# Kernel tuning notes

Hardware: AMD Instinct MI355X
Metric: run time of the kernel (lower is better)

The kernel has to match this reference:

```python
import jax, jax.numpy as jnp
import numpy as np

N, E, R = 50000, 1600000, 8
IN_F, HID_F, OUT_F = 128, 64, 64


def setup_inputs() -> dict:
    key = jax.random.key(0)
    ks = jax.random.split(key, 9)
    x = jax.random.normal(ks[0], (N, IN_F), dtype=jnp.float32)
    edge_index = jax.random.randint(ks[1], (2, E), 0, N, dtype=jnp.int64)
    edge_type = jax.random.randint(ks[2], (E,), 0, R, dtype=jnp.int64)
    # layer 1 params (scaled like glorot)
    s1 = 1.0 / np.sqrt(IN_F)
    W1_rel = jax.random.normal(ks[3], (R, IN_F, HID_F), dtype=jnp.float32) * s1
    W1_root = jax.random.normal(ks[4], (IN_F, HID_F), dtype=jnp.float32) * s1
    b1 = jnp.zeros((HID_F,), dtype=jnp.float32)
    # layer 2 params
    s2 = 1.0 / np.sqrt(HID_F)
    W2_rel = jax.random.normal(ks[5], (R, HID_F, OUT_F), dtype=jnp.float32) * s2
    W2_root = jax.random.normal(ks[6], (HID_F, OUT_F), dtype=jnp.float32) * s2
    b2 = jnp.zeros((OUT_F,), dtype=jnp.float32)
    return {"x": x, "edge_index": edge_index, "edge_type": edge_type,
            "W1_rel": W1_rel, "W1_root": W1_root, "b1": b1,
            "W2_rel": W2_rel, "W2_root": W2_root, "b2": b2}


def _rgcn_conv(x, src, dst, etype, W_rel, W_root, b):
    """PyG RGCNConv: root transform + per-relation mean-aggregated messages."""
    n = x.shape[0]
    r = W_rel.shape[0]
    # per-relation transform of all node features: [R, N, H]
    xw = jnp.einsum('nd,rdh->rnh', x, W_rel)
    # per-edge message: transformed source feature under the edge's relation
    msg = xw[etype, src]  # [E, H]
    # mean normalization per (dst, relation) pair
    key = dst * r + etype  # [E]
    cnt = jax.ops.segment_sum(jnp.ones(etype.shape, dtype=x.dtype), key,
                              num_segments=n * r)
    inv = 1.0 / jnp.maximum(cnt, 1.0)
    msg = msg * inv[key][:, None]
    # scatter-add into target nodes
    agg = jax.ops.segment_sum(msg, dst, num_segments=n)  # [N, H]
    return agg + x @ W_root + b


def reference(x, edge_index, edge_type, W1_rel, W1_root, b1, W2_rel, W2_root, b2):
    src, dst = edge_index[0], edge_index[1]
    h = _rgcn_conv(x, src, dst, edge_type, W1_rel, W1_root, b1)
    h = jax.nn.relu(h)
    out = _rgcn_conv(h, src, dst, edge_type, W2_rel, W2_root, b2)
    return out
```

## Files before the change

kernel.cpp:

```cpp
#include <hip/hip_runtime.h>


constexpr int NN  = 50000;
constexpr int NE  = 1600000;
constexpr int NR  = 8;
constexpr int FIN = 128;
constexpr int FH  = 64;

constexpr int BSH = 7;
constexpr int BN  = 1 << BSH;
constexpr int NB  = (NN + BN - 1) >> BSH;
constexpr int CAP = 6144;
constexpr int CH  = 4096;
constexpr unsigned XWMAX = (unsigned)(NN - 1) * (NR * 64) + (NR - 1) * 64;

typedef __attribute__((ext_vector_type(8))) short bf16x8;
typedef __attribute__((ext_vector_type(4))) float f32x4;

__device__ __forceinline__ unsigned short f2bf(float f) {
  unsigned u = __float_as_uint(f);
  u = (u + 0x7fff + ((u >> 16) & 1)) >> 16;
  return (unsigned short)u;
}
__device__ __forceinline__ float bf2f(unsigned short b) {
  return __uint_as_float(((unsigned)b) << 16);
}
__device__ __forceinline__ bool edge_ok(unsigned s, unsigned d, unsigned r) {
  return s < NN && d < NN && r < NR;
}

__global__ void __launch_bounds__(256) bucket_append(
    const int* __restrict__ src, const int* __restrict__ dst,
    const int* __restrict__ et, int* __restrict__ bcur,
    unsigned* __restrict__ brecs) {
  __shared__ uint2 stage[CH];
  __shared__ int h[NB], gbase[NB], sbase[NB], scur[NB];
  __shared__ int wtot[4];
  const int t  = threadIdx.x;
  const int c0 = blockIdx.x * CH;
  const int m  = min(CH, NE - c0);

  for (int i = t; i < NB; i += 256) h[i] = 0;
  __syncthreads();

  for (int i = t; i < m; i += 256) {
    const unsigned s = (unsigned)src[c0 + i];
    const unsigned d = (unsigned)dst[c0 + i];
    const unsigned r = (unsigned)et[c0 + i];
    if (edge_ok(s, d, r)) atomicAdd(&h[d >> BSH], 1);
  }
  __syncthreads();

  const int v0 = (2 * t < NB) ? h[2 * t] : 0;
  const int v1 = (2 * t + 1 < NB) ? h[2 * t + 1] : 0;
  if (2 * t < NB     && v0) gbase[2 * t]     = atomicAdd(&bcur[2 * t], v0);
  if (2 * t + 1 < NB && v1) gbase[2 * t + 1] = atomicAdd(&bcur[2 * t + 1], v1);
  const int s = v0 + v1;
  int incl = s;
#pragma unroll
  for (int o = 1; o < 64; o <<= 1) {
    int u = __shfl_up(incl, o, 64);
    if ((t & 63) >= o) incl += u;
  }
  if ((t & 63) == 63) wtot[t >> 6] = incl;
  __syncthreads();
  int wo = 0;
  for (int w = 0; w < (t >> 6); ++w) wo += wtot[w];
  const int e = wo + incl - s;
  if (2 * t < NB)     { sbase[2 * t] = e;          scur[2 * t] = e; }
  if (2 * t + 1 < NB) { sbase[2 * t + 1] = e + v0; scur[2 * t + 1] = e + v0; }
  __syncthreads();

  for (int i = t; i < m; i += 256) {
    const unsigned sv = (unsigned)src[c0 + i];
    const unsigned d  = (unsigned)dst[c0 + i];
    const unsigned r  = (unsigned)et[c0 + i];
    if (edge_ok(sv, d, r)) {
      const int p = atomicAdd(&scur[d >> BSH], 1);
      if (p < CH) stage[p] = make_uint2((sv << 10) | (((unsigned)d & (BN - 1)) << 3) | r, d);
    }
  }
  __syncthreads();

  const int M = min(sbase[NB - 1] + h[NB - 1], CH);
  for (int j = t; j < M; j += 256) {
    const uint2 rec = stage[j];
    const int b = (int)(rec.y >> BSH);
    const int idx = min(gbase[b] + (j - sbase[b]), NB * CAP - 1);
    brecs[idx] = rec.x;
  }
}

__global__ void __launch_bounds__(256) bucket_finalize(
    const int* __restrict__ bcur, const unsigned* __restrict__ brecs,
    float* __restrict__ inv, int* __restrict__ row_start,
    int* __restrict__ deg, unsigned* __restrict__ recs) {
  const int b    = blockIdx.x;
  const int base = b * CAP;
  const int m    = min(bcur[b] - base, CAP);
  const int d0   = b << BSH;
  __shared__ int cnt[BN * NR];
  __shared__ int curs[BN * NR];
  __shared__ int wtot[4];
  const int t = threadIdx.x;

  for (int i = t; i < BN * NR; i += 256) cnt[i] = 0;
  __syncthreads();
  for (int i = t; i < m; i += 256) {
    const unsigned rec = brecs[base + i];
    const int dl = (int)((rec >> 3) & (BN - 1));
    const int r  = (int)(rec & 7);
    atomicAdd(&cnt[dl * NR + r], 1);
  }
  __syncthreads();

  const int c0 = cnt[t * 4], c1 = cnt[t * 4 + 1], c2 = cnt[t * 4 + 2], c3 = cnt[t * 4 + 3];
  const int s = c0 + c1 + c2 + c3;
  int incl = s;
#pragma unroll
  for (int o = 1; o < 64; o <<= 1) {
    int u = __shfl_up(incl, o, 64);
    if ((t & 63) >= o) incl += u;
  }
  if ((t & 63) == 63) wtot[t >> 6] = incl;
  __syncthreads();
  int wo = 0;
  for (int w = 0; w < (t >> 6); ++w) wo += wtot[w];
  const int e = wo + incl - s;
  curs[t * 4]     = e;
  curs[t * 4 + 1] = e + c0;
  curs[t * 4 + 2] = e + c0 + c1;
  curs[t * 4 + 3] = e + c0 + c1 + c2;
  __syncthreads();

  if (t < BN) {
    const int d = d0 + t;
    if (d < NN) {
      const int start = curs[t * NR];
      const int end   = (t == BN - 1) ? m : curs[(t + 1) * NR];
      row_start[d] = base + start;
      deg[d]       = end - start;
#pragma unroll
      for (int r = 0; r < NR; ++r)
        inv[d * NR + r] = 1.0f / fmaxf((float)cnt[t * NR + r], 1.0f);
    }
  }
  __syncthreads();

  for (int i = t; i < m; i += 256) {
    const unsigned rec = brecs[base + i];
    const int dl = (int)((rec >> 3) & (BN - 1));
    const int r  = (int)(rec & 7);
    const unsigned sv = rec >> 10;
    const int p  = atomicAdd(&curs[dl * NR + r], 1);
    recs[base + min(p, CAP - 1)] = (sv << 9) | ((unsigned)r << 6);
  }
}

__global__ void prep(const float* __restrict__ W1r, const float* __restrict__ W1o,
                     const float* __restrict__ W2r, const float* __restrict__ W2o,
                     unsigned short* __restrict__ Wt1,
                     unsigned short* __restrict__ Wt2,
                     int* __restrict__ bcur) {
  const int i  = blockIdx.x * blockDim.x + threadIdx.x;
  if (i < NB) bcur[i] = i * CAP;
  const int n1 = (NR + 1) * 64 * FIN;
  const int n2 = (NR + 1) * 64 * FH;
  if (i < n1) {
    const int g = i / (64 * FIN), rem = i % (64 * FIN);
    const int n = rem / FIN, k = rem % FIN;
    const float* W = (g < NR) ? (W1r + (size_t)g * FIN * 64) : W1o;
    Wt1[i] = f2bf(W[k * 64 + n]);
  } else if (i < n1 + n2) {
    const int j = i - n1;
    const int g = j / (64 * FH), rem = j % (64 * FH);
    const int n = rem / FH, k = rem % FH;
    const float* W = (g < NR) ? (W2r + (size_t)g * FH * 64) : W2o;
    Wt2[j] = f2bf(W[k * 64 + n]);
  }
}

template <int K, bool A_FP32>
__global__ void __launch_bounds__(256) gemm_mfma(
    const void* __restrict__ Av, const unsigned short* __restrict__ Wt,
    const float* __restrict__ bias,
    unsigned short* __restrict__ xw, float* __restrict__ root_out) {
  constexpr int KP  = K + 8;
  constexpr int NCH = 64 * (K / 8) / 256;
  __shared__ unsigned short As[64 * KP];
  __shared__ unsigned short Bs[2][64 * KP];
  const int n0  = blockIdx.x * 64;
  const int tid = threadIdx.x;

  if constexpr (A_FP32) {
    const float* A = (const float*)Av;
    for (int c = tid; c < 64 * (K / 8); c += 256) {
      const int row = c / (K / 8), kp = (c % (K / 8)) * 8;
      bf16x8 v = {};
      if (n0 + row < NN) {
        const float* p = A + (size_t)(n0 + row) * K + kp;
        const float4 f0 = *(const float4*)p;
        const float4 f1 = *(const float4*)(p + 4);
        v[0] = f2bf(f0.x); v[1] = f2bf(f0.y); v[2] = f2bf(f0.z); v[3] = f2bf(f0.w);
        v[4] = f2bf(f1.x); v[5] = f2bf(f1.y); v[6] = f2bf(f1.z); v[7] = f2bf(f1.w);
      }
      *(bf16x8*)(As + row * KP + kp) = v;
    }
  } else {
    const unsigned short* A = (const unsigned short*)Av;
    for (int c = tid; c < 64 * (K / 8); c += 256) {
      const int row = c / (K / 8), kp = (c % (K / 8)) * 8;
      bf16x8 v = {};
      if (n0 + row < NN) v = *(const bf16x8*)(A + (size_t)(n0 + row) * K + kp);
      *(bf16x8*)(As + row * KP + kp) = v;
    }
  }

  for (int c = 0; c < NCH; ++c) {
    const int idx = tid + c * 256;
    const int row = idx / (K / 8), kp = (idx % (K / 8)) * 8;
    *(bf16x8*)(Bs[0] + row * KP + kp) = *(const bf16x8*)(Wt + idx * 8);
  }
  __syncthreads();

  const int wave = tid >> 6, lane = tid & 63;
  const int i16 = lane & 15, quad = lane >> 4;
  const int r0 = wave * 16 + i16;

  for (int g = 0; g <= NR; ++g) {
    const int buf = g & 1;
    bf16x8 breg[NCH];
    if (g < NR) {
      const unsigned short* Wn = Wt + (size_t)(g + 1) * 64 * K;
#pragma unroll
      for (int c = 0; c < NCH; ++c) breg[c] = *(const bf16x8*)(Wn + (tid + c * 256) * 8);
    }

    f32x4 acc[4] = {};
#pragma unroll
    for (int kc = 0; kc < K / 32; ++kc) {
      const int k0 = kc * 32 + quad * 8;
      const bf16x8 a0 = *(const bf16x8*)(As + r0 * KP + k0);
      const bf16x8 b0 = *(const bf16x8*)(Bs[buf] + (i16)      * KP + k0);
      const bf16x8 b1 = *(const bf16x8*)(Bs[buf] + (i16 + 16) * KP + k0);
      const bf16x8 b2 = *(const bf16x8*)(Bs[buf] + (i16 + 32) * KP + k0);
      const bf16x8 b3 = *(const bf16x8*)(Bs[buf] + (i16 + 48) * KP + k0);
      acc[0] = __builtin_amdgcn_mfma_f32_16x16x32_bf16(a0, b0, acc[0], 0, 0, 0);
      acc[1] = __builtin_amdgcn_mfma_f32_16x16x32_bf16(a0, b1, acc[1], 0, 0, 0);
      acc[2] = __builtin_amdgcn_mfma_f32_16x16x32_bf16(a0, b2, acc[2], 0, 0, 0);
      acc[3] = __builtin_amdgcn_mfma_f32_16x16x32_bf16(a0, b3, acc[3], 0, 0, 0);
    }

    if (g < NR) {
#pragma unroll
      for (int c = 0; c < NCH; ++c) {
        const int idx = tid + c * 256;
        const int row = idx / (K / 8), kp = (idx % (K / 8)) * 8;
        *(bf16x8*)(Bs[buf ^ 1] + row * KP + kp) = breg[c];
      }
    }

    if (g < NR) {
#pragma unroll
      for (int reg = 0; reg < 4; ++reg) {
        const int n = n0 + wave * 16 + quad * 4 + reg;
        if (n >= NN) continue;
        unsigned short* p = xw + (size_t)n * (NR * 64) + g * 64 + i16;
#pragma unroll
        for (int ct = 0; ct < 4; ++ct) p[ct * 16] = f2bf(acc[ct][reg]);
      }
    } else {
      float bv[4];
#pragma unroll
      for (int ct = 0; ct < 4; ++ct) bv[ct] = bias[ct * 16 + i16];
#pragma unroll
      for (int reg = 0; reg < 4; ++reg) {
        const int n = n0 + wave * 16 + quad * 4 + reg;
        if (n >= NN) continue;
        float* p = root_out + (size_t)n * 64 + i16;
#pragma unroll
        for (int ct = 0; ct < 4; ++ct) p[ct * 16] = acc[ct][reg] + bv[ct];
      }
    }
    __syncthreads();
  }
}

template <bool RELU_BF16>
__global__ void __launch_bounds__(256) agg_csr(
    const int* __restrict__ row_start, const int* __restrict__ deg,
    const unsigned* __restrict__ offs, const unsigned short* __restrict__ xw,
    const float* __restrict__ inv, const float* __restrict__ root,
    float* __restrict__ out_f32, unsigned short* __restrict__ out_b16) {
  const int gid  = blockIdx.x * blockDim.x + threadIdx.x;
  const int lane = gid & 63;
  const int d    = gid >> 6;
  if (d >= NN) return;
  const int e  = lane >> 3;
  const int l8 = lane & 7;
  const int base = row_start[d];
  const int n    = deg[d];
  const float invv = inv[(d << 3) + l8];
  float a[8] = {};

  for (int c = 0; c < n; c += 64) {
    const int m = min(64, n - c);
    unsigned off = 0;
    if (lane < m) off = offs[base + c + lane];
    for (int j = 0; j < m; j += 16) {
      const int i0 = j + e, i1 = j + 8 + e;
      unsigned u0 = __shfl(off, i0 & 63, 64);
      unsigned u1 = __shfl(off, i1 & 63, 64);
      float s0 = __shfl(invv, (int)((u0 >> 6) & 7), 64);
      float s1 = __shfl(invv, (int)((u1 >> 6) & 7), 64);
      u0 = min(u0, XWMAX); u1 = min(u1, XWMAX);
      if (i0 >= m) s0 = 0.f;
      if (i1 >= m) s1 = 0.f;
      const bf16x8 v0 = *(const bf16x8*)(xw + u0 + l8 * 8);
      const bf16x8 v1 = *(const bf16x8*)(xw + u1 + l8 * 8);
#pragma unroll
      for (int q = 0; q < 8; ++q) a[q] += bf2f((unsigned short)v0[q]) * s0;
#pragma unroll
      for (int q = 0; q < 8; ++q) a[q] += bf2f((unsigned short)v1[q]) * s1;
    }
  }

#pragma unroll
  for (int q = 0; q < 8; ++q) {
    a[q] += __shfl_xor(a[q], 8, 64);
    a[q] += __shfl_xor(a[q], 16, 64);
    a[q] += __shfl_xor(a[q], 32, 64);
  }

  if (e == 0) {
    const float4 r0 = *(const float4*)(root + (size_t)d * 64 + l8 * 8);
    const float4 r1 = *(const float4*)(root + (size_t)d * 64 + l8 * 8 + 4);
    const float o[8] = {r0.x + a[0], r0.y + a[1], r0.z + a[2], r0.w + a[3],
                        r1.x + a[4], r1.y + a[5], r1.z + a[6], r1.w + a[7]};
    if (RELU_BF16) {
      bf16x8 ov;
#pragma unroll
      for (int q = 0; q < 8; ++q) ov[q] = (short)f2bf(fmaxf(o[q], 0.f));
      *(bf16x8*)(out_b16 + (size_t)d * 64 + l8 * 8) = ov;
    } else {
      *(float4*)(out_f32 + (size_t)d * 64 + l8 * 8)     = make_float4(o[0], o[1], o[2], o[3]);
      *(float4*)(out_f32 + (size_t)d * 64 + l8 * 8 + 4) = make_float4(o[4], o[5], o[6], o[7]);
    }
  }
}

extern "C" void kernel_launch(void* const* d_in, const int* in_sizes, int n_in,
                              void* d_out, int out_size, void* d_ws, size_t ws_size,
                              hipStream_t stream) {
  const float* x   = (const float*)d_in[0];
  const int*   ei  = (const int*)d_in[1];
  const int*   et  = (const int*)d_in[2];
  const float* W1r = (const float*)d_in[3];
  const float* W1o = (const float*)d_in[4];
  const float* b1  = (const float*)d_in[5];
  const float* W2r = (const float*)d_in[6];
  const float* W2o = (const float*)d_in[7];
  const float* b2  = (const float*)d_in[8];
  float* out = (float*)d_out;

  const int* src = ei;
  const int* dst = ei + NE;

  char* ws = (char*)d_ws;
  size_t off = 0;
  auto alloc = [&](size_t bytes) {
    void* p = ws + off; off += (bytes + 255) & ~(size_t)255; return p;
  };
  int*   bcur      = (int*)alloc((size_t)NB * 4);
  float* inv       = (float*)alloc((size_t)NN * NR * 4);
  int*   row_start = (int*)alloc((size_t)NN * 4);
  int*   deg       = (int*)alloc((size_t)NN * 4);
  unsigned* brecs  = (unsigned*)alloc((size_t)NB * CAP * 4);
  unsigned* offs   = (unsigned*)alloc((size_t)NB * CAP * 4);
  unsigned short* xw    = (unsigned short*)alloc((size_t)NN * NR * 64 * 2);
  unsigned short* hb    = (unsigned short*)alloc((size_t)NN * FH * 2);
  float*          hroot = (float*)alloc((size_t)NN * 64 * 4);
  unsigned short* Wt1   = (unsigned short*)alloc((size_t)(NR + 1) * 64 * FIN * 2);
  unsigned short* Wt2   = (unsigned short*)alloc((size_t)(NR + 1) * 64 * FH * 2);

  const int nprep = (NR + 1) * 64 * (FIN + FH);
  prep<<<(nprep + 255) / 256, 256, 0, stream>>>(W1r, W1o, W2r, W2o, Wt1, Wt2, bcur);
  bucket_append<<<(NE + CH - 1) / CH, 256, 0, stream>>>(src, dst, et, bcur, brecs);
  bucket_finalize<<<NB, 256, 0, stream>>>(bcur, brecs, inv, row_start, deg, offs);

  const int gemm_blocks = (NN + 63) / 64;
  const int agg_blocks  = (NN * 64 + 255) / 256;
  gemm_mfma<FIN, true><<<gemm_blocks, 256, 0, stream>>>(x, Wt1, b1, xw, hroot);
  agg_csr<true><<<agg_blocks, 256, 0, stream>>>(row_start, deg, offs, xw, inv, hroot, nullptr, hb);
  gemm_mfma<FH, false><<<gemm_blocks, 256, 0, stream>>>(hb, Wt2, b2, xw, out);
  agg_csr<false><<<agg_blocks, 256, 0, stream>>>(row_start, deg, offs, xw, inv, out, out, nullptr);
}
```

Measured before the change: 253.7 us.

## Fuse bucket append with layer-1 GEMM and pack counts into edge records

The edge bucketing kernel and the first GEMM become one launch, with blocks split by index, so the two independent phases overlap and one launch is saved. The per-(dst,relation) count is packed into the top bits of each CSR record, which removes the inv array. The aggregation kernel now loads records directly per lane with four independent gathers per iteration instead of shuffling offsets and weights. This risks larger shared-memory use in the fused kernel, approximate reciprocals, and a count saturating at 127.

```diff
diff --git a/kernel.cpp b/kernel.cpp
--- a/kernel.cpp
+++ b/kernel.cpp
@@ -12,6 +12,7 @@
 constexpr int NB  = (NN + BN - 1) >> BSH;
 constexpr int CAP = 6144;
 constexpr int CH  = 4096;
+constexpr int NAPP = (NE + CH - 1) / CH;
 constexpr unsigned XWMAX = (unsigned)(NN - 1) * (NR * 64) + (NR - 1) * 64;
 
 typedef __attribute__((ext_vector_type(8))) short bf16x8;
@@ -29,15 +30,21 @@
   return s < NN && d < NN && r < NR;
 }
 
-__global__ void __launch_bounds__(256) bucket_append(
-    const int* __restrict__ src, const int* __restrict__ dst,
-    const int* __restrict__ et, int* __restrict__ bcur,
-    unsigned* __restrict__ brecs) {
-  __shared__ uint2 stage[CH];
-  __shared__ int h[NB], gbase[NB], sbase[NB], scur[NB];
-  __shared__ int wtot[4];
+__device__ void append_body(char* smem, int bx,
+                            const int* __restrict__ src,
+                            const int* __restrict__ dst,
+                            const int* __restrict__ et,
+                            int* __restrict__ bcur,
+                            unsigned* __restrict__ brecs) {
+  uint2* stage = (uint2*)smem;
+  int* h     = (int*)(smem + (size_t)CH * 8);
+  int* gbase = h + NB;
+  int* sbase = gbase + NB;
+  int* scur  = sbase + NB;
+  int* wtot  = scur + NB;
+
   const int t  = threadIdx.x;
-  const int c0 = blockIdx.x * CH;
+  const int c0 = bx * CH;
   const int m  = min(CH, NE - c0);
 
   for (int i = t; i < NB; i += 256) h[i] = 0;
@@ -93,8 +100,8 @@
 
 __global__ void __launch_bounds__(256) bucket_finalize(
     const int* __restrict__ bcur, const unsigned* __restrict__ brecs,
-    float* __restrict__ inv, int* __restrict__ row_start,
-    int* __restrict__ deg, unsigned* __restrict__ recs) {
+    int* __restrict__ row_start, int* __restrict__ deg,
+    unsigned* __restrict__ recs) {
   const int b    = blockIdx.x;
   const int base = b * CAP;
   const int m    = min(bcur[b] - base, CAP);
@@ -140,9 +147,6 @@
       const int end   = (t == BN - 1) ? m : curs[(t + 1) * NR];
       row_start[d] = base + start;
       deg[d]       = end - start;
-#pragma unroll
-      for (int r = 0; r < NR; ++r)
-        inv[d * NR + r] = 1.0f / fmaxf((float)cnt[t * NR + r], 1.0f);
     }
   }
   __syncthreads();
@@ -153,7 +157,8 @@
     const int r  = (int)(rec & 7);
     const unsigned sv = rec >> 10;
     const int p  = atomicAdd(&curs[dl * NR + r], 1);
-    recs[base + min(p, CAP - 1)] = (sv << 9) | ((unsigned)r << 6);
+    const unsigned cn = (unsigned)min(cnt[dl * NR + r], 127);
+    recs[base + min(p, CAP - 1)] = (cn << 25) | (sv << 9) | ((unsigned)r << 6);
   }
 }
 
@@ -181,15 +186,17 @@
 }
 
 template <int K, bool A_FP32>
-__global__ void __launch_bounds__(256) gemm_mfma(
-    const void* __restrict__ Av, const unsigned short* __restrict__ Wt,
-    const float* __restrict__ bias,
-    unsigned short* __restrict__ xw, float* __restrict__ root_out) {
+__device__ void gemm_body(char* smem, int bx,
+                          const void* __restrict__ Av,
+                          const unsigned short* __restrict__ Wt,
+                          const float* __restrict__ bias,
+                          unsigned short* __restrict__ xw,
+                          float* __restrict__ root_out) {
   constexpr int KP  = K + 8;
   constexpr int NCH = 64 * (K / 8) / 256;
-  __shared__ unsigned short As[64 * KP];
-  __shared__ unsigned short Bs[2][64 * KP];
-  const int n0  = blockIdx.x * 64;
+  unsigned short* As  = (unsigned short*)smem;
+  unsigned short* Bs0 = As + 64 * KP;
+  const int n0  = bx * 64;
   const int tid = threadIdx.x;
 
   if constexpr (A_FP32) {
@@ -219,7 +226,7 @@
   for (int c = 0; c < NCH; ++c) {
     const int idx = tid + c * 256;
     const int row = idx / (K / 8), kp = (idx % (K / 8)) * 8;
-    *(bf16x8*)(Bs[0] + row * KP + kp) = *(const bf16x8*)(Wt + idx * 8);
+    *(bf16x8*)(Bs0 + row * KP + kp) = *(const bf16x8*)(Wt + idx * 8);
   }
   __syncthreads();
 
@@ -229,6 +236,8 @@
 
   for (int g = 0; g <= NR; ++g) {
     const int buf = g & 1;
+    unsigned short* Bc = Bs0 + buf * 64 * KP;
+    unsigned short* Bn = Bs0 + (buf ^ 1) * 64 * KP;
     bf16x8 breg[NCH];
     if (g < NR) {
       const unsigned short* Wn = Wt + (size_t)(g + 1) * 64 * K;
@@ -241,10 +250,10 @@
     for (int kc = 0; kc < K / 32; ++kc) {
       const int k0 = kc * 32 + quad * 8;
       const bf16x8 a0 = *(const bf16x8*)(As + r0 * KP + k0);
-      const bf16x8 b0 = *(const bf16x8*)(Bs[buf] + (i16)      * KP + k0);
-      const bf16x8 b1 = *(const bf16x8*)(Bs[buf] + (i16 + 16) * KP + k0);
-      const bf16x8 b2 = *(const bf16x8*)(Bs[buf] + (i16 + 32) * KP + k0);
-      const bf16x8 b3 = *(const bf16x8*)(Bs[buf] + (i16 + 48) * KP + k0);
+      const bf16x8 b0 = *(const bf16x8*)(Bc + (i16)      * KP + k0);
+      const bf16x8 b1 = *(const bf16x8*)(Bc + (i16 + 16) * KP + k0);
+      const bf16x8 b2 = *(const bf16x8*)(Bc + (i16 + 32) * KP + k0);
+      const bf16x8 b3 = *(const bf16x8*)(Bc + (i16 + 48) * KP + k0);
       acc[0] = __builtin_amdgcn_mfma_f32_16x16x32_bf16(a0, b0, acc[0], 0, 0, 0);
       acc[1] = __builtin_amdgcn_mfma_f32_16x16x32_bf16(a0, b1, acc[1], 0, 0, 0);
       acc[2] = __builtin_amdgcn_mfma_f32_16x16x32_bf16(a0, b2, acc[2], 0, 0, 0);
@@ -256,7 +265,7 @@
       for (int c = 0; c < NCH; ++c) {
         const int idx = tid + c * 256;
         const int row = idx / (K / 8), kp = (idx % (K / 8)) * 8;
-        *(bf16x8*)(Bs[buf ^ 1] + row * KP + kp) = breg[c];
+        *(bf16x8*)(Bn + row * KP + kp) = breg[c];
       }
     }
 
@@ -286,11 +295,33 @@
   }
 }
 
+__global__ void __launch_bounds__(256) fused_append_gemm1(
+    const int* __restrict__ src, const int* __restrict__ dst,
+    const int* __restrict__ et, int* __restrict__ bcur,
+    unsigned* __restrict__ brecs,
+    const float* __restrict__ A, const unsigned short* __restrict__ Wt,
+    const float* __restrict__ bias, unsigned short* __restrict__ xw,
+    float* __restrict__ root_out) {
+  extern __shared__ char smem[];
+  if ((int)blockIdx.x < NAPP)
+    append_body(smem, (int)blockIdx.x, src, dst, et, bcur, brecs);
+  else
+    gemm_body<FIN, true>(smem, (int)blockIdx.x - NAPP, A, Wt, bias, xw, root_out);
+}
+
+__global__ void __launch_bounds__(256) gemm_l2(
+    const unsigned short* __restrict__ A, const unsigned short* __restrict__ Wt,
+    const float* __restrict__ bias, unsigned short* __restrict__ xw,
+    float* __restrict__ out) {
+  extern __shared__ char smem[];
+  gemm_body<FH, false>(smem, (int)blockIdx.x, A, Wt, bias, xw, out);
+}
+
 template <bool RELU_BF16>
 __global__ void __launch_bounds__(256) agg_csr(
     const int* __restrict__ row_start, const int* __restrict__ deg,
-    const unsigned* __restrict__ offs, const unsigned short* __restrict__ xw,
-    const float* __restrict__ inv, const float* __restrict__ root,
+    const unsigned* __restrict__ recs, const unsigned short* __restrict__ xw,
+    const float* __restrict__ root,
     float* __restrict__ out_f32, unsigned short* __restrict__ out_b16) {
   const int gid  = blockIdx.x * blockDim.x + threadIdx.x;
   const int lane = gid & 63;
@@ -300,29 +331,40 @@
   const int l8 = lane & 7;
   const int base = row_start[d];
   const int n    = deg[d];
-  const float invv = inv[(d << 3) + l8];
+  const unsigned* po = recs + base;
+  const unsigned short* xp = xw + l8 * 8;
   float a[8] = {};
 
-  for (int c = 0; c < n; c += 64) {
-    const int m = min(64, n - c);
-    unsigned off = 0;
-    if (lane < m) off = offs[base + c + lane];
-    for (int j = 0; j < m; j += 16) {
-      const int i0 = j + e, i1 = j + 8 + e;
-      unsigned u0 = __shfl(off, i0 & 63, 64);
-      unsigned u1 = __shfl(off, i1 & 63, 64);
-      float s0 = __shfl(invv, (int)((u0 >> 6) & 7), 64);
-      float s1 = __shfl(invv, (int)((u1 >> 6) & 7), 64);
-      u0 = min(u0, XWMAX); u1 = min(u1, XWMAX);
-      if (i0 >= m) s0 = 0.f;
-      if (i1 >= m) s1 = 0.f;
-      const bf16x8 v0 = *(const bf16x8*)(xw + u0 + l8 * 8);
-      const bf16x8 v1 = *(const bf16x8*)(xw + u1 + l8 * 8);
-#pragma unroll
-      for (int q = 0; q < 8; ++q) a[q] += bf2f((unsigned short)v0[q]) * s0;
-#pragma unroll
-      for (int q = 0; q < 8; ++q) a[q] += bf2f((unsigned short)v1[q]) * s1;
-    }
+  for (int i0 = 0; i0 < n; i0 += 32) {
+    const int i = i0 + e;
+    const unsigned r0 = (i      < n) ? po[i]      : 0u;
+    const unsigned r1 = (i + 8  < n) ? po[i + 8]  : 0u;
+    const unsigned r2 = (i + 16 < n) ? po[i + 16] : 0u;
+    const unsigned r3 = (i + 24 < n) ? po[i + 24] : 0u;
+    const unsigned u0 = min(r0 & 0x01FFFFFFu, XWMAX);
+    const unsigned u1 = min(r1 & 0x01FFFFFFu, XWMAX);
+    const unsigned u2 = min(r2 & 0x01FFFFFFu, XWMAX);
+    const unsigned u3 = min(r3 & 0x01FFFFFFu, XWMAX);
+    const bf16x8 v0 = *(const bf16x8*)(xp + u0);
+    const bf16x8 v1 = *(const bf16x8*)(xp + u1);
+    const bf16x8 v2 = *(const bf16x8*)(xp + u2);
+    const bf16x8 v3 = *(const bf16x8*)(xp + u3);
+    float w0 = __builtin_amdgcn_rcpf((float)(r0 >> 25));
+    float w1 = __builtin_amdgcn_rcpf((float)(r1 >> 25));
+    float w2 = __builtin_amdgcn_rcpf((float)(r2 >> 25));
+    float w3 = __builtin_amdgcn_rcpf((float)(r3 >> 25));
+    if (i      >= n) w0 = 0.f;
+    if (i + 8  >= n) w1 = 0.f;
+    if (i + 16 >= n) w2 = 0.f;
+    if (i + 24 >= n) w3 = 0.f;
+#pragma unroll
+    for (int q = 0; q < 8; ++q) a[q] += bf2f((unsigned short)v0[q]) * w0;
+#pragma unroll
+    for (int q = 0; q < 8; ++q) a[q] += bf2f((unsigned short)v1[q]) * w1;
+#pragma unroll
+    for (int q = 0; q < 8; ++q) a[q] += bf2f((unsigned short)v2[q]) * w2;
+#pragma unroll
+    for (int q = 0; q < 8; ++q) a[q] += bf2f((unsigned short)v3[q]) * w3;
   }
 
 #pragma unroll
@@ -372,7 +414,6 @@
     void* p = ws + off; off += (bytes + 255) & ~(size_t)255; return p;
   };
   int*   bcur      = (int*)alloc((size_t)NB * 4);
-  float* inv       = (float*)alloc((size_t)NN * NR * 4);
   int*   row_start = (int*)alloc((size_t)NN * 4);
   int*   deg       = (int*)alloc((size_t)NN * 4);
   unsigned* brecs  = (unsigned*)alloc((size_t)NB * CAP * 4);
@@ -385,13 +426,17 @@
 
   const int nprep = (NR + 1) * 64 * (FIN + FH);
   prep<<<(nprep + 255) / 256, 256, 0, stream>>>(W1r, W1o, W2r, W2o, Wt1, Wt2, bcur);
-  bucket_append<<<(NE + CH - 1) / CH, 256, 0, stream>>>(src, dst, et, bcur, brecs);
-  bucket_finalize<<<NB, 256, 0, stream>>>(bcur, brecs, inv, row_start, deg, offs);
 
   const int gemm_blocks = (NN + 63) / 64;
   const int agg_blocks  = (NN * 64 + 255) / 256;
-  gemm_mfma<FIN, true><<<gemm_blocks, 256, 0, stream>>>(x, Wt1, b1, xw, hroot);
-  agg_csr<true><<<agg_blocks, 256, 0, stream>>>(row_start, deg, offs, xw, inv, hroot, nullptr, hb);
-  gemm_mfma<FH, false><<<gemm_blocks, 256, 0, stream>>>(hb, Wt2, b2, xw, out);
-  agg_csr<false><<<agg_blocks, 256, 0, stream>>>(row_start, deg, offs, xw, inv, out, out, nullptr);
-}
+  constexpr int SM1 = 3 * 64 * (FIN + 8) * 2;
+  constexpr int SM2 = 3 * 64 * (FH + 8) * 2;
+
+  fused_append_gemm1<<<NAPP + gemm_blocks, 256, SM1, stream>>>(
+      src, dst, et, bcur, brecs, x, Wt1, b1, xw, hroot);
+  bucket_finalize<<<NB, 256, 0, stream>>>(bcur, brecs, row_start, deg, offs);
+
+  agg_csr<true><<<agg_blocks, 256, 0, stream>>>(row_start, deg, offs, xw, hroot, nullptr, hb);
+  gemm_l2<<<gemm_blocks, 256, SM2, stream>>>(hb, Wt2, b2, xw, out);
+  agg_csr<false><<<agg_blocks, 256, 0, stream>>>(row_start, deg, offs, xw, out, out, nullptr);
+}
```

Measured after the change: 243.3 us. 1.04x faster.
